# Performance work log

Measured on AMD Instinct MI355X. Metric: run time of the kernel, lower is better.

The kernel has to match this reference:

```python
import jax, jax.numpy as jnp
import numpy as np

EPS_RMS = 1e-6
EPS_NORM = 1e-9


def rmsnorm(x):
    return x * jax.lax.rsqrt(jnp.mean(x * x, axis=-1, keepdims=True) + EPS_RMS)


def apply_rotary(x, cos, sin):
    # x: [b, h, s, d]; cos/sin: [1, 1, s, d//2]
    d2 = x.shape[-1] // 2
    x1, x2 = x[..., :d2], x[..., d2:]
    return jnp.concatenate([x1 * cos - x2 * sin, x1 * sin + x2 * cos], axis=-1)


def setup_inputs() -> dict:
    key = jax.random.key(0)
    ks = jax.random.split(key, 16)
    b, l, e, h = 4, 1024, 2048, 16
    d = e // h
    query = jax.random.normal(ks[0], (b, l, e), jnp.float32)
    keyt = jax.random.normal(ks[1], (b, l, e), jnp.float32)
    value = jax.random.normal(ks[2], (b, l, e), jnp.float32)
    attn_mask = jnp.tril(jnp.ones((l, l), bool))[None, None]  # causal bool mask
    cos = jax.random.normal(ks[3], (1, 1, l, d // 2), jnp.float32)
    sin = jax.random.normal(ks[4], (1, 1, l, d // 2), jnp.float32)
    sc = 0.02
    Wq = jax.random.normal(ks[5], (e, e), jnp.float32) * sc
    bq = jnp.zeros((e,), jnp.float32)
    Wk = jax.random.normal(ks[6], (e, e), jnp.float32) * sc
    bk = jnp.zeros((e,), jnp.float32)
    Wv = jax.random.normal(ks[7], (e, e), jnp.float32) * sc
    bv = jnp.zeros((e,), jnp.float32)
    Wo = jax.random.normal(ks[8], (e, e), jnp.float32) * sc
    bo = jnp.zeros((e,), jnp.float32)
    return dict(query=query, key=keyt, value=value, attn_mask=attn_mask,
                cos=cos, sin=sin, Wq=Wq, bq=bq, Wk=Wk, bk=bk,
                Wv=Wv, bv=bv, Wo=Wo, bo=bo)


def reference(query, key, value, attn_mask, cos, sin, Wq, bq, Wk, bk, Wv, bv, Wo, bo):
    b, l, e = query.shape
    s = key.shape[1]
    h = 16
    d = e // h
    q = (query @ Wq.T + bq).reshape(b, l, h, d).transpose(0, 2, 1, 3)
    k = (key @ Wk.T + bk).reshape(b, s, h, d).transpose(0, 2, 1, 3)
    v = (value @ Wv.T + bv).reshape(b, s, h, d).transpose(0, 2, 1, 3)
    q, k = rmsnorm(q), rmsnorm(k)
    # rotary (self-attention, s == l)
    q = apply_rotary(q, cos[:, :, :s], sin[:, :, :s])
    k = apply_rotary(k, cos[:, :, :s], sin[:, :, :s])
    # SDPA with boolean mask
    scores = jnp.einsum('bhld,bhsd->bhls', q, k) / jnp.sqrt(jnp.float32(d))
    scores = jnp.where(attn_mask, scores, jnp.finfo(scores.dtype).min)
    p = jax.nn.softmax(scores, axis=-1)
    o = jnp.einsum('bhls,bhsd->bhld', p, v)  # [b,h,l,d]
    # post-attention v-orthogonalization (o.shape == v.shape here)
    vnorm = jnp.sqrt(jnp.sum(v * v, axis=-1, keepdims=True))
    vn = v / jnp.maximum(vnorm, EPS_NORM)
    o = o - jnp.sum(o * vn, axis=-1, keepdims=True) * vn
    o = o.transpose(0, 2, 1, 3).reshape(b, l, e)
    return o @ Wo.T + bo
```

## Files before the change

### kernel.cpp

```cpp
#include <hip/hip_runtime.h>

typedef short short8 __attribute__((ext_vector_type(8)));
typedef float f32x4 __attribute__((ext_vector_type(4)));

#define MFMA_BF16 __builtin_amdgcn_mfma_f32_16x16x32_bf16

__device__ __forceinline__ unsigned short f2bf(float f) {
  unsigned int u = __float_as_uint(f);
  u += 0x7fffu + ((u >> 16) & 1u);
  return (unsigned short)(u >> 16);
}
__device__ __forceinline__ float bf2f(unsigned short u) {
  return __uint_as_float(((unsigned int)u) << 16);
}

typedef __attribute__((address_space(1))) const unsigned int as1_u32;
typedef __attribute__((address_space(3))) unsigned int as3_u32;
__device__ __forceinline__ void gld16(const void* g, void* l) {
  __builtin_amdgcn_global_load_lds((as1_u32*)(unsigned long long)g,
                                   (as3_u32*)(unsigned int)(unsigned long long)l,
                                   16, 0, 0);
}

template <int N>
__device__ __forceinline__ void vmwait() {
  if constexpr (N == 0) asm volatile("s_waitcnt vmcnt(0)" ::: "memory");
  else if constexpr (N == 4) asm volatile("s_waitcnt vmcnt(4)" ::: "memory");
  else if constexpr (N == 6) asm volatile("s_waitcnt vmcnt(6)" ::: "memory");
}
__device__ __forceinline__ void barrier_raw() {
  asm volatile("" ::: "memory");
  __builtin_amdgcn_s_barrier();
  asm volatile("" ::: "memory");
}

struct CvtArgs {
  const float* s[7];
  unsigned short* d[7];
  int n8[7];
};

__global__ __launch_bounds__(256) void cvtall(CvtArgs a) {
  const int seg = blockIdx.y;
  int i = blockIdx.x * 256 + threadIdx.x;
  if (i >= a.n8[seg]) return;
  const float4* s4 = (const float4*)a.s[seg];
  float4 x = s4[2 * i], y = s4[2 * i + 1];
  short8 o = {(short)f2bf(x.x), (short)f2bf(x.y), (short)f2bf(x.z), (short)f2bf(x.w),
              (short)f2bf(y.x), (short)f2bf(y.y), (short)f2bf(y.z), (short)f2bf(y.w)};
  *(short8*)&a.d[seg][(size_t)i * 8] = o;
}

struct GemmArgs {
  const unsigned short* A[3];
  const unsigned short* W[3];
  const float* bias[3];
  unsigned short* Cb[3];
  float* Cf;
};

template <bool OUTBF, int NZ, int MF>
__global__ __launch_bounds__(256, 2) void gemm_bf16(GemmArgs g) {
  extern __shared__ unsigned short Sh[];
  constexpr int NA = MF / 2;
  constexpr int L = NA + 2;
  constexpr int MH = MF / 2;
  constexpr int BOFF = MF * 1024;
  constexpr int RS = MF * 1024 + 4096;
  const int K = 2048, N = 2048, NT = 64;

  const int B = blockIdx.x;
  int z, bm, bn;
  if constexpr (MF == 8) {
    z = B >> 8;
    const int i = B & 255;
    const int xcd = i & 7, q = i >> 3;
    bm = (xcd * 2 + (q & 1)) * 256;
    bn = (q >> 1) * 128;
  } else {
    z = 0;
    const int xcd = B & 7, q = B >> 3;
    bm = (xcd * 4 + (q & 3)) * 128;
    bn = (q >> 2) * 128;
  }

  const unsigned short* __restrict__ A = g.A[z];
  const unsigned short* __restrict__ W = g.W[z];
  const float* __restrict__ bias = g.bias[z];
  unsigned short* __restrict__ Cb = g.Cb[z];

  const int t = threadIdx.x, lane = t & 63, w = t >> 6;
  const int wr = w >> 1, wc = w & 1;
  const int quad = lane >> 4, l16 = lane & 15;

  const int sk = ((lane & 3) * 8) ^ (((lane >> 3) & 3) << 3);
  const int srow = lane >> 2;
  size_t gA[NA], gB[2];
  int lA[NA], lB[2];
  for (int j = 0; j < NA; ++j) {
    gA[j] = (size_t)(bm + w * (MF * 8) + j * 16 + srow) * K + sk;
    lA[j] = (w * (MF * 8) + j * 16) * 32;
  }
  for (int j = 0; j < 2; ++j) {
    gB[j] = (size_t)(bn + w * 32 + j * 16 + srow) * K + sk;
    lB[j] = BOFF + (w * 32 + j * 16) * 32;
  }

  auto STAGE_A = [&](int kq, unsigned short* Ld) {
    for (int j = 0; j < NA; ++j) gld16(A + gA[j] + kq, Ld + lA[j]);
  };
  auto STAGE_B = [&](int kq, unsigned short* Ld) {
    for (int j = 0; j < 2; ++j) gld16(W + gB[j] + kq, Ld + lB[j]);
  };

  const int ka = (quad * 8) ^ (((l16 >> 1) & 3) << 3);
  const int raA = (wr * (MF * 16) + l16) * 32 + ka;
  const int raB = BOFF + (wc * 64 + l16) * 32 + ka;

  const f32x4 fz = {0.f, 0.f, 0.f, 0.f};
  f32x4 acc[MF][4];
  for (int a = 0; a < MF; ++a)
    for (int b = 0; b < 4; ++b) acc[a][b] = fz;

  unsigned short* cur = Sh;
  unsigned short* nxt = Sh + RS;
  unsigned short* stg = Sh + 2 * RS;

  STAGE_A(0, cur);  STAGE_B(0, cur);
  STAGE_A(32, nxt); STAGE_B(32, nxt);
  vmwait<L>();
  barrier_raw();

  for (int tt = 0; tt < NT; ++tt) {
    short8 af0[MH], bv[4];
#pragma unroll
    for (int mt = 0; mt < MH; ++mt)
      af0[mt] = *(const short8*)&cur[raA + mt * 512];
#pragma unroll
    for (int nt = 0; nt < 4; ++nt)
      bv[nt] = *(const short8*)&cur[raB + nt * 512];
    if (tt + 2 < NT) STAGE_A((tt + 2) * 32, stg);
    barrier_raw();
    __builtin_amdgcn_s_setprio(1);
#pragma unroll
    for (int mt = 0; mt < MH; ++mt)
#pragma unroll
      for (int nt = 0; nt < 4; ++nt)
        acc[mt][nt] = MFMA_BF16(af0[mt], bv[nt], acc[mt][nt], 0, 0, 0);
    __builtin_amdgcn_s_setprio(0);
    barrier_raw();

    short8 af1[MH];
#pragma unroll
    for (int mt = 0; mt < MH; ++mt)
      af1[mt] = *(const short8*)&cur[raA + (MH + mt) * 512];
    if (tt + 2 < NT) STAGE_B((tt + 2) * 32, stg);
    if (tt < NT - 2) vmwait<L>();
    else if (tt == NT - 2) vmwait<0>();
    barrier_raw();
    __builtin_amdgcn_s_setprio(1);
#pragma unroll
    for (int mt = 0; mt < MH; ++mt)
#pragma unroll
      for (int nt = 0; nt < 4; ++nt)
        acc[MH + mt][nt] = MFMA_BF16(af1[mt], bv[nt], acc[MH + mt][nt], 0, 0, 0);
    __builtin_amdgcn_s_setprio(0);
    barrier_raw();

    unsigned short* tmp = cur; cur = nxt; nxt = stg; stg = tmp;
  }

  for (int mt = 0; mt < MF; ++mt)
    for (int nt = 0; nt < 4; ++nt) {
      int row = bm + wr * (MF * 16) + mt * 16 + quad * 4;
      int col = bn + wc * 64 + nt * 16 + l16;
      float bc = bias[col];
      for (int r2 = 0; r2 < 4; ++r2) {
        float v = acc[mt][nt][r2] + bc;
        if (OUTBF) Cb[(size_t)(row + r2) * N + col] = f2bf(v);
        else       g.Cf[(size_t)(row + r2) * N + col] = v;
      }
    }
}

__global__ __launch_bounds__(256) void rmsvt(
    const unsigned short* __restrict__ Qf, const unsigned short* __restrict__ Kf,
    const unsigned short* __restrict__ Vf,
    const float* __restrict__ cosT, const float* __restrict__ sinT,
    unsigned short* __restrict__ Qb, unsigned short* __restrict__ Kb,
    unsigned short* __restrict__ Vt) {
  __shared__ unsigned short Vsh[64 * 136];
  if (blockIdx.x < 16384) {
    const int rid = blockIdx.x * 4 + (threadIdx.x >> 6);
    const int lane = threadIdx.x & 63;
    const int li = rid & 1023;
    const int bh = rid >> 10;
    const int hi = bh & 15, bi = bh >> 4;
    const int src = (bi * 1024 + li) * 2048 + hi * 128;
    const int dst = rid * 128;
    const float c = cosT[li * 64 + lane];
    const float s = sinT[li * 64 + lane];

    float q1 = bf2f(Qf[src + lane]), q2 = bf2f(Qf[src + 64 + lane]);
    float ss = q1 * q1 + q2 * q2;
    for (int off = 32; off; off >>= 1) ss += __shfl_xor(ss, off, 64);
    float r = rsqrtf(ss * (1.f / 128.f) + 1e-6f);
    float qa = q1 * r, qb2 = q2 * r;
    const float qsc = 0.08838834764831845f * 1.4426950408889634f;
    Qb[dst + lane]      = f2bf((qa * c - qb2 * s) * qsc);
    Qb[dst + 64 + lane] = f2bf((qa * s + qb2 * c) * qsc);

    float k1 = bf2f(Kf[src + lane]), k2 = bf2f(Kf[src + 64 + lane]);
    float ks = k1 * k1 + k2 * k2;
    for (int off = 32; off; off >>= 1) ks += __shfl_xor(ks, off, 64);
    float rk = rsqrtf(ks * (1.f / 128.f) + 1e-6f);
    float ka = k1 * rk, kb2 = k2 * rk;
    Kb[dst + lane]      = f2bf(ka * c - kb2 * s);
    Kb[dst + 64 + lane] = f2bf(ka * s + kb2 * c);
  } else {
    const int bid = blockIdx.x - 16384;
    const int t = threadIdx.x;
    const int bh = bid >> 4, l0 = (bid & 15) * 64;
    const int hi = bh & 15, bi = bh >> 4;
    {
      int row = t >> 2, c4 = t & 3;
      const unsigned short* src = &Vf[(size_t)(bi * 1024 + l0 + row) * 2048 + hi * 128];
      for (int i = 0; i < 4; ++i) {
        int chunk = c4 * 4 + i;
        *(int4*)&Vsh[row * 136 + chunk * 8] = *(const int4*)&src[chunk * 8];
      }
    }
    __syncthreads();
    {
      int d = t >> 1, half = t & 1;
      unsigned short* dst = &Vt[(size_t)bh * 131072 + (size_t)d * 1024 + l0 + half * 32];
      for (int g = 0; g < 4; ++g) {
        short8 o;
        for (int j = 0; j < 8; ++j)
          o[j] = (short)Vsh[(half * 32 + g * 8 + j) * 136 + d];
        *(short8*)&dst[g * 8] = o;
      }
    }
  }
}

__global__ __launch_bounds__(512, 4) void attn(
    const unsigned short* __restrict__ Qb, const unsigned short* __restrict__ Kb,
    const unsigned short* __restrict__ Vt, unsigned short* __restrict__ Of0,
    unsigned short* __restrict__ Of1, float* __restrict__ Lb) {
  __shared__ unsigned short Pl[8][16 * 72];
  const int t = threadIdx.x, lane = t & 63, w = t >> 6;
  const int quad = lane >> 4, l16 = lane & 15;
  const int B = blockIdx.x;
  const int bh = (B & 7) + 8 * ((B >> 3) & 7);
  const int jj = B >> 6;
  const int pair = jj >> 1, split = jj & 1;
  const unsigned short* Qh = Qb + (size_t)bh * 131072;
  const unsigned short* Kh = Kb + (size_t)bh * 131072;
  const unsigned short* Vh = Vt + (size_t)bh * 131072;
  unsigned short* Oh = (split ? Of1 : Of0) + (size_t)bh * 131072;
  float* Lh = Lb + split * 65536 + bh * 1024;

  const f32x4 fz = {0.f, 0.f, 0.f, 0.f};

  for (int ti = 0; ti < 2; ++ti) {
    const int qt = ti == 0 ? 7 - pair : pair;
    const int q0 = qt * 128;

    short8 aQ[4];
    {
      int qr = q0 + w * 16 + l16;
      for (int kk = 0; kk < 4; ++kk)
        aQ[kk] = *(const short8*)&Qh[(size_t)qr * 128 + kk * 32 + quad * 8];
    }
    f32x4 oacc[8];
    for (int i = 0; i < 8; ++i) oacc[i] = fz;
    float Lr[4] = {0.f, 0.f, 0.f, 0.f};
    const int nST = 2 * qt + 2;

    for (int st = split; st < nST; st += 2) {
      const int s0 = st * 64;

      f32x4 sfr[4];
      for (int j = 0; j < 4; ++j) sfr[j] = fz;
#pragma unroll
      for (int kk = 0; kk < 4; ++kk)
#pragma unroll
        for (int ni = 0; ni < 4; ++ni) {
          short8 bK = *(const short8*)&Kh[(size_t)(s0 + ni * 16 + l16) * 128 +
                                          kk * 32 + quad * 8];
          sfr[ni] = MFMA_BF16(aQ[kk], bK, sfr[ni], 0, 0, 0);
        }

      const bool diag = (s0 + 63 > q0);
      for (int r = 0; r < 4; ++r) {
        int q = q0 + w * 16 + quad * 4 + r;
        float ps = 0.f;
        for (int ni = 0; ni < 4; ++ni) {
          float sv = sfr[ni][r];
          if (diag && (s0 + ni * 16 + l16 > q)) sv = -30000.f;
          float pp = exp2f(sv - 16.5f);
          ps += pp;
          Pl[w][(quad * 4 + r) * 72 + ni * 16 + l16] = f2bf(pp);
        }
        ps += __shfl_xor(ps, 1, 64);
        ps += __shfl_xor(ps, 2, 64);
        ps += __shfl_xor(ps, 4, 64);
        ps += __shfl_xor(ps, 8, 64);
        Lr[r] += ps;
      }

#pragma unroll
      for (int kk = 0; kk < 2; ++kk) {
        short8 aP = *(const short8*)&Pl[w][l16 * 72 + kk * 32 + quad * 8];
#pragma unroll
        for (int nt = 0; nt < 8; ++nt) {
          short8 bV = *(const short8*)&Vh[(size_t)(nt * 16 + l16) * 1024 +
                                          s0 + kk * 32 + quad * 8];
          oacc[nt] = MFMA_BF16(aP, bV, oacc[nt], 0, 0, 0);
        }
      }
    }

    for (int r = 0; r < 4; ++r) {
      int q = q0 + w * 16 + quad * 4 + r;
      size_t base = (size_t)q * 128;
      for (int nt = 0; nt < 8; ++nt)
        Oh[base + nt * 16 + l16] = f2bf(oacc[nt][r]);
      if (l16 == 0) Lh[q] = Lr[r];
    }
  }
}

__global__ __launch_bounds__(256) void vnfix(
    const unsigned short* __restrict__ Of0, const unsigned short* __restrict__ Of1,
    const float* __restrict__ Lb, const unsigned short* __restrict__ Vf,
    unsigned short* __restrict__ Op) {
  const int rid = blockIdx.x * 4 + (threadIdx.x >> 6);
  const int lane = threadIdx.x & 63;
  const int li = rid & 1023;
  const int bh = rid >> 10;
  const int hi = bh & 15, bi = bh >> 4;
  const int src = (bi * 1024 + li) * 2048 + hi * 128;
  float inv = 1.f / (Lb[rid] + Lb[65536 + rid]);
  float o1 = (bf2f(Of0[(size_t)rid * 128 + lane]) + bf2f(Of1[(size_t)rid * 128 + lane])) * inv;
  float o2 = (bf2f(Of0[(size_t)rid * 128 + 64 + lane]) + bf2f(Of1[(size_t)rid * 128 + 64 + lane])) * inv;
  float v1 = bf2f(Vf[src + lane]), v2 = bf2f(Vf[src + 64 + lane]);
  float vv = v1 * v1 + v2 * v2;
  float dd = o1 * v1 + o2 * v2;
  for (int off = 32; off; off >>= 1) {
    vv += __shfl_xor(vv, off, 64);
    dd += __shfl_xor(dd, off, 64);
  }
  float vn = fmaxf(sqrtf(vv), 1e-9f);
  float tc = dd / (vn * vn);
  Op[src + lane]      = f2bf(o1 - tc * v1);
  Op[src + 64 + lane] = f2bf(o2 - tc * v2);
}

extern "C" void kernel_launch(void* const* d_in, const int* in_sizes, int n_in,
                              void* d_out, int out_size, void* d_ws, size_t ws_size,
                              hipStream_t stream) {
  const float* query = (const float*)d_in[0];
  const float* key   = (const float*)d_in[1];
  const float* value = (const float*)d_in[2];
  const float* cosT  = (const float*)d_in[4];
  const float* sinT  = (const float*)d_in[5];
  const float* Wq = (const float*)d_in[6];
  const float* bq = (const float*)d_in[7];
  const float* Wk = (const float*)d_in[8];
  const float* bk = (const float*)d_in[9];
  const float* Wv = (const float*)d_in[10];
  const float* bv = (const float*)d_in[11];
  const float* Wo = (const float*)d_in[12];
  const float* bo = (const float*)d_in[13];
  float* out = (float*)d_out;

  char* ws = (char*)d_ws;
  const size_t MB = 1048576;
  unsigned short* Xq  = (unsigned short*)(ws);
  unsigned short* Xk  = (unsigned short*)(ws + 16 * MB);
  unsigned short* Xv  = (unsigned short*)(ws + 32 * MB);
  unsigned short* Wqb = (unsigned short*)(ws + 48 * MB);
  unsigned short* Wkb = (unsigned short*)(ws + 56 * MB);
  unsigned short* Wvb = (unsigned short*)(ws + 64 * MB);
  unsigned short* Wob = (unsigned short*)(ws + 72 * MB);
  unsigned short* Qf  = (unsigned short*)(ws + 80 * MB);
  unsigned short* Kf  = (unsigned short*)(ws + 96 * MB);
  unsigned short* Vf  = (unsigned short*)(ws + 112 * MB);
  unsigned short* Qbb = Xq;
  unsigned short* Kbb = Xk;
  unsigned short* Vtb = Xv;
  unsigned short* Of0 = Qf;
  unsigned short* Of1 = Kf;
  float*          Lbp = (float*)(ws + 64 * MB);
  unsigned short* Opb = (unsigned short*)(ws + 48 * MB);

  CvtArgs ca;
  ca.s[0] = query; ca.d[0] = Xq;  ca.n8[0] = 1048576;
  ca.s[1] = key;   ca.d[1] = Xk;  ca.n8[1] = 1048576;
  ca.s[2] = value; ca.d[2] = Xv;  ca.n8[2] = 1048576;
  ca.s[3] = Wq;    ca.d[3] = Wqb; ca.n8[3] = 524288;
  ca.s[4] = Wk;    ca.d[4] = Wkb; ca.n8[4] = 524288;
  ca.s[5] = Wv;    ca.d[5] = Wvb; ca.n8[5] = 524288;
  ca.s[6] = Wo;    ca.d[6] = Wob; ca.n8[6] = 524288;
  cvtall<<<dim3(4096, 7), 256, 0, stream>>>(ca);

  GemmArgs gp;
  gp.A[0] = Xq;  gp.A[1] = Xk;  gp.A[2] = Xv;
  gp.W[0] = Wqb; gp.W[1] = Wkb; gp.W[2] = Wvb;
  gp.bias[0] = bq; gp.bias[1] = bk; gp.bias[2] = bv;
  gp.Cb[0] = Qf; gp.Cb[1] = Kf; gp.Cb[2] = Vf;
  gp.Cf = nullptr;
  gemm_bf16<true, 3, 8><<<768, 256, 73728, stream>>>(gp);

  rmsvt<<<17408, 256, 0, stream>>>(Qf, Kf, Vf, cosT, sinT, Qbb, Kbb, Vtb);

  attn<<<512, 512, 0, stream>>>(Qbb, Kbb, Vtb, Of0, Of1, Lbp);

  vnfix<<<16384, 256, 0, stream>>>(Of0, Of1, Lbp, Vf, Opb);

  GemmArgs go;
  go.A[0] = Opb; go.A[1] = nullptr; go.A[2] = nullptr;
  go.W[0] = Wob; go.W[1] = nullptr; go.W[2] = nullptr;
  go.bias[0] = bo; go.bias[1] = nullptr; go.bias[2] = nullptr;
  go.Cb[0] = nullptr; go.Cb[1] = nullptr; go.Cb[2] = nullptr;
  go.Cf = out;
  gemm_bf16<false, 1, 4><<<512, 256, 49152, stream>>>(go);
}
```

Baseline: 513.6 us.

## Stage K/V tiles in LDS with double buffering and larger query tiles

The attention kernel now loads K and V tiles into swizzled shared memory with async global-to-LDS copies and double buffering. Each wave now handles 32 query rows instead of 16, so one staged tile serves twice the rows and the grid shrinks from 512 to 256 blocks. The intent is to cut redundant global/L2 reads of K and V, which were previously fetched straight from global memory by every wave. The output GEMM also switches to a larger tile with fewer blocks. The cost is lower occupancy (launch bounds 2, 100KB LDS) and fewer blocks to fill the GPU.

```diff
diff --git a/kernel.cpp b/kernel.cpp
--- a/kernel.cpp
+++ b/kernel.cpp
@@ -244,91 +244,152 @@
   }
 }
 
-__global__ __launch_bounds__(512, 4) void attn(
+__global__ __launch_bounds__(512, 2) void attn(
     const unsigned short* __restrict__ Qb, const unsigned short* __restrict__ Kb,
     const unsigned short* __restrict__ Vt, unsigned short* __restrict__ Of0,
     unsigned short* __restrict__ Of1, float* __restrict__ Lb) {
-  __shared__ unsigned short Pl[8][16 * 72];
+  extern __shared__ unsigned short Sh[];
   const int t = threadIdx.x, lane = t & 63, w = t >> 6;
   const int quad = lane >> 4, l16 = lane & 15;
   const int B = blockIdx.x;
   const int bh = (B & 7) + 8 * ((B >> 3) & 7);
-  const int jj = B >> 6;
-  const int pair = jj >> 1, split = jj & 1;
+  const int p = (B >> 6) & 1, split = (B >> 7) & 1;
   const unsigned short* Qh = Qb + (size_t)bh * 131072;
   const unsigned short* Kh = Kb + (size_t)bh * 131072;
   const unsigned short* Vh = Vt + (size_t)bh * 131072;
   unsigned short* Oh = (split ? Of1 : Of0) + (size_t)bh * 131072;
   float* Lh = Lb + split * 65536 + bh * 1024;
-
+  unsigned short* Pw = Sh + 32768 + w * 2304;
+
+  const int kc = (lane & 15) * 8;
+  const int vcc = (lane & 7) * 8;
   const f32x4 fz = {0.f, 0.f, 0.f, 0.f};
 
+  auto STAGE = [&](int s0, int buf) {
+    unsigned short* Kd = Sh + buf * 8192;
+    unsigned short* Vd = Sh + 16384 + buf * 8192;
+#pragma unroll
+    for (int j = 0; j < 2; ++j) {
+      int row = w * 8 + 4 * j + (lane >> 4);
+      int sc = kc ^ ((row & 7) << 3);
+      gld16(&Kh[(size_t)(s0 + row) * 128 + sc], &Kd[(w * 8 + 4 * j) * 128]);
+    }
+#pragma unroll
+    for (int j = 0; j < 2; ++j) {
+      int row = w * 16 + 8 * j + (lane >> 3);
+      int sc = vcc ^ ((row & 7) << 3);
+      gld16(&Vh[(size_t)row * 1024 + s0 + sc], &Vd[(w * 16 + 8 * j) * 64]);
+    }
+  };
+
   for (int ti = 0; ti < 2; ++ti) {
-    const int qt = ti == 0 ? 7 - pair : pair;
-    const int q0 = qt * 128;
-
-    short8 aQ[4];
-    {
-      int qr = q0 + w * 16 + l16;
+    const int qt = ti == 0 ? 3 - p : p;
+    const int q0 = qt * 256;
+    const int qw = q0 + w * 32;
+
+    short8 aQ[2][4];
+#pragma unroll
+    for (int rt = 0; rt < 2; ++rt) {
+      int qr = qw + rt * 16 + l16;
+#pragma unroll
       for (int kk = 0; kk < 4; ++kk)
-        aQ[kk] = *(const short8*)&Qh[(size_t)qr * 128 + kk * 32 + quad * 8];
-    }
-    f32x4 oacc[8];
-    for (int i = 0; i < 8; ++i) oacc[i] = fz;
-    float Lr[4] = {0.f, 0.f, 0.f, 0.f};
-    const int nST = 2 * qt + 2;
-
-    for (int st = split; st < nST; st += 2) {
-      const int s0 = st * 64;
-
-      f32x4 sfr[4];
-      for (int j = 0; j < 4; ++j) sfr[j] = fz;
-#pragma unroll
-      for (int kk = 0; kk < 4; ++kk)
-#pragma unroll
-        for (int ni = 0; ni < 4; ++ni) {
-          short8 bK = *(const short8*)&Kh[(size_t)(s0 + ni * 16 + l16) * 128 +
-                                          kk * 32 + quad * 8];
-          sfr[ni] = MFMA_BF16(aQ[kk], bK, sfr[ni], 0, 0, 0);
+        aQ[rt][kk] = *(const short8*)&Qh[(size_t)qr * 128 + kk * 32 + quad * 8];
+    }
+    f32x4 oacc[2][8];
+#pragma unroll
+    for (int rt = 0; rt < 2; ++rt)
+#pragma unroll
+      for (int i = 0; i < 8; ++i) oacc[rt][i] = fz;
+    float Lr[2][4] = {{0.f, 0.f, 0.f, 0.f}, {0.f, 0.f, 0.f, 0.f}};
+    const int n = 2 * qt + 2;
+
+    vmwait<0>();
+    barrier_raw();
+    STAGE(split * 64, 0);
+
+    for (int i = 0; i < n; ++i) {
+      const int s0 = (split + 2 * i) * 64;
+      barrier_raw();
+      if (i + 1 < n) {
+        STAGE((split + 2 * (i + 1)) * 64, (i + 1) & 1);
+        vmwait<4>();
+      } else {
+        vmwait<0>();
+      }
+      barrier_raw();
+      const unsigned short* Kl = Sh + (i & 1) * 8192;
+      const unsigned short* Vl = Sh + 16384 + (i & 1) * 8192;
+
+      f32x4 sfr[2][4];
+#pragma unroll
+      for (int rt = 0; rt < 2; ++rt)
+#pragma unroll
+        for (int ni = 0; ni < 4; ++ni) sfr[rt][ni] = fz;
+#pragma unroll
+      for (int kk = 0; kk < 4; ++kk) {
+        short8 bK[4];
+#pragma unroll
+        for (int ni = 0; ni < 4; ++ni)
+          bK[ni] = *(const short8*)&Kl[(ni * 16 + l16) * 128 +
+                                       ((kk * 32 + quad * 8) ^ ((l16 & 7) << 3))];
+#pragma unroll
+        for (int rt = 0; rt < 2; ++rt)
+#pragma unroll
+          for (int ni = 0; ni < 4; ++ni)
+            sfr[rt][ni] = MFMA_BF16(aQ[rt][kk], bK[ni], sfr[rt][ni], 0, 0, 0);
+      }
+
+#pragma unroll
+      for (int rt = 0; rt < 2; ++rt) {
+        const bool diag = (s0 + 63 > qw + rt * 16);
+#pragma unroll
+        for (int r = 0; r < 4; ++r) {
+          int q = qw + rt * 16 + quad * 4 + r;
+          float ps = 0.f;
+#pragma unroll
+          for (int ni = 0; ni < 4; ++ni) {
+            float sv = sfr[rt][ni][r];
+            if (diag && (s0 + ni * 16 + l16 > q)) sv = -30000.f;
+            float pp = exp2f(sv - 16.5f);
+            ps += pp;
+            Pw[(rt * 16 + quad * 4 + r) * 72 + ni * 16 + l16] = f2bf(pp);
+          }
+          ps += __shfl_xor(ps, 1, 64);
+          ps += __shfl_xor(ps, 2, 64);
+          ps += __shfl_xor(ps, 4, 64);
+          ps += __shfl_xor(ps, 8, 64);
+          Lr[rt][r] += ps;
         }
-
-      const bool diag = (s0 + 63 > q0);
+      }
+
+#pragma unroll
+      for (int kk = 0; kk < 2; ++kk) {
+        short8 aP[2];
+#pragma unroll
+        for (int rt = 0; rt < 2; ++rt)
+          aP[rt] = *(const short8*)&Pw[(rt * 16 + l16) * 72 + kk * 32 + quad * 8];
+#pragma unroll
+        for (int nt = 0; nt < 8; ++nt) {
+          short8 bV = *(const short8*)&Vl[(nt * 16 + l16) * 64 +
+                                          ((kk * 32 + quad * 8) ^ ((l16 & 7) << 3))];
+#pragma unroll
+          for (int rt = 0; rt < 2; ++rt)
+            oacc[rt][nt] = MFMA_BF16(aP[rt], bV, oacc[rt][nt], 0, 0, 0);
+        }
+      }
+    }
+
+#pragma unroll
+    for (int rt = 0; rt < 2; ++rt)
+#pragma unroll
       for (int r = 0; r < 4; ++r) {
-        int q = q0 + w * 16 + quad * 4 + r;
-        float ps = 0.f;
-        for (int ni = 0; ni < 4; ++ni) {
-          float sv = sfr[ni][r];
-          if (diag && (s0 + ni * 16 + l16 > q)) sv = -30000.f;
-          float pp = exp2f(sv - 16.5f);
-          ps += pp;
-          Pl[w][(quad * 4 + r) * 72 + ni * 16 + l16] = f2bf(pp);
-        }
-        ps += __shfl_xor(ps, 1, 64);
-        ps += __shfl_xor(ps, 2, 64);
-        ps += __shfl_xor(ps, 4, 64);
-        ps += __shfl_xor(ps, 8, 64);
-        Lr[r] += ps;
-      }
-
-#pragma unroll
-      for (int kk = 0; kk < 2; ++kk) {
-        short8 aP = *(const short8*)&Pl[w][l16 * 72 + kk * 32 + quad * 8];
-#pragma unroll
-        for (int nt = 0; nt < 8; ++nt) {
-          short8 bV = *(const short8*)&Vh[(size_t)(nt * 16 + l16) * 1024 +
-                                          s0 + kk * 32 + quad * 8];
-          oacc[nt] = MFMA_BF16(aP, bV, oacc[nt], 0, 0, 0);
-        }
-      }
-    }
-
-    for (int r = 0; r < 4; ++r) {
-      int q = q0 + w * 16 + quad * 4 + r;
-      size_t base = (size_t)q * 128;
-      for (int nt = 0; nt < 8; ++nt)
-        Oh[base + nt * 16 + l16] = f2bf(oacc[nt][r]);
-      if (l16 == 0) Lh[q] = Lr[r];
-    }
+        int q = qw + rt * 16 + quad * 4 + r;
+        size_t base = (size_t)q * 128;
+#pragma unroll
+        for (int nt = 0; nt < 8; ++nt)
+          Oh[base + nt * 16 + l16] = f2bf(oacc[rt][nt][r]);
+        if (l16 == 0) Lh[q] = Lr[rt][r];
+      }
   }
 }
 
@@ -416,7 +477,7 @@
 
   rmsvt<<<17408, 256, 0, stream>>>(Qf, Kf, Vf, cosT, sinT, Qbb, Kbb, Vtb);
 
-  attn<<<512, 512, 0, stream>>>(Qbb, Kbb, Vtb, Of0, Of1, Lbp);
+  attn<<<256, 512, 102400, stream>>>(Qbb, Kbb, Vtb, Of0, Of1, Lbp);
 
   vnfix<<<16384, 256, 0, stream>>>(Of0, Of1, Lbp, Vf, Opb);
 
@@ -426,5 +487,5 @@
   go.bias[0] = bo; go.bias[1] = nullptr; go.bias[2] = nullptr;
   go.Cb[0] = nullptr; go.Cb[1] = nullptr; go.Cb[2] = nullptr;
   go.Cf = out;
-  gemm_bf16<false, 1, 4><<<512, 256, 49152, stream>>>(go);
-}
+  gemm_bf16<false, 1, 8><<<256, 256, 73728, stream>>>(go);
+}
```

New measurement: 432.1 us. 15.9% less time.
